# Optimization experiments

Measured on AMD Instinct MI355X. Metric: run time of the kernel, lower is better.

## Reference

```python
import jax, jax.numpy as jnp
from jax import lax
import numpy as np

B, T, N = 32, 1024, 128


def setup_inputs() -> dict:
    key = jax.random.key(0)
    k1, k2, k3 = jax.random.split(key, 3)
    x = jax.random.normal(k1, (B, T, N), dtype=jnp.float32)
    w_init = jax.random.normal(k2, (B, N, N), dtype=jnp.float32)
    mask = jax.random.randint(k3, (B, T), 0, 2, dtype=jnp.int32)
    alpha = jnp.float32(0.9)
    eta = jnp.float32(0.01)
    return {"x": x, "w_init": w_init, "alpha": alpha, "eta": eta, "mask": mask}


def reference(x, w_init, alpha, eta, mask):
    # x: (B,T,N), w_init: (B,N,N), mask: (B,T) int {0,1}
    maskf = mask.astype(x.dtype)

    def step(w, inp):
        xt, mt = inp                       # (B,N), (B,)
        yt = jnp.einsum('bij,bj->bi', w, xt)           # read-out with OLD w
        outer = xt[:, :, None] * xt[:, None, :]        # (B,N,N) Hebbian outer product
        w_new = alpha * w + eta * outer                # decay + Hebbian update
        m = mt[:, None, None]
        w = m * w_new + (1.0 - m) * w                  # masked update
        return w, yt

    xs = jnp.swapaxes(x, 0, 1)     # (T,B,N)
    ms = jnp.swapaxes(maskf, 0, 1) # (T,B)
    w_final, ys = lax.scan(step, w_init, (xs, ms))
    y_seq = jnp.swapaxes(ys, 0, 1)  # (B,T,N)
    return w_final, y_seq
```

## Files before the change

kernel.cpp:

```cpp
#include <hip/hip_runtime.h>

#define BB 32
#define TT 1024
#define NN 128
#define YB 256

#define ROR_ADD(p, ctrl)                                                      \
  p += __int_as_float(__builtin_amdgcn_update_dpp(                            \
      0, __float_as_int(p), ctrl, 0xF, 0xF, true));
#define BCAST15_ADD(p)                                                        \
  p += __int_as_float(__builtin_amdgcn_update_dpp(                            \
      0, __float_as_int(p), 0x142, 0xF, 0xF, true));

__global__ __launch_bounds__(256)
void bdh_seq_kernel(const float* __restrict__ x,
                    const float* __restrict__ w_init,
                    const float* __restrict__ alpha_p,
                    const float* __restrict__ eta_p,
                    const int*   __restrict__ mask,
                    float* __restrict__ out)
{
    const int tid  = threadIdx.x;
    const int bidx = blockIdx.x;
    const int b      = bidx & 31;
    const int i_base = (bidx >> 5) << 3;
    const int rloc   = tid >> 5;
    const int i      = i_base + rloc;
    const int cg     = tid & 31;
    const int j0     = cg << 2;

    __shared__ float ybuf[YB][8];

    const float alpha = alpha_p[0];
    const float eta   = eta_p[0];

    const float* xb   = x + (size_t)b * TT * NN;
    const float* xcol = xb + j0;
    const int*   mb   = mask + b * TT;

    float* wout = out + ((size_t)b * NN + i) * NN + j0;
    float* yout = out + (size_t)BB * NN * NN + (size_t)b * TT * NN;

    float4 w = *reinterpret_cast<const float4*>(
        w_init + ((size_t)b * NN + i) * NN + j0);

    float4 XA = *reinterpret_cast<const float4*>(xcol + 0 * NN);
    float4 XB = *reinterpret_cast<const float4*>(xcol + 1 * NN);
    float4 XC = *reinterpret_cast<const float4*>(xcol + 2 * NN);
    float4 XD = *reinterpret_cast<const float4*>(xcol + 3 * NN);
    float xiA = xb[0 * NN + i], xiB = xb[1 * NN + i];
    float xiC = xb[2 * NN + i], xiD = xb[3 * NN + i];
    int   mA_ = mb[0], mB_ = mb[1], mC_ = mb[2], mD_ = mb[3];

#define STEP(tt, X, XI, MM, TNEXT)                                            \
  {                                                                           \
    const float aa = MM ? alpha : 1.0f;                                       \
    const float ci = (MM ? eta : 0.0f) * XI;                                  \
      \
    float p0 = fmaf(w.y, X.y, w.x * X.x);                                     \
    float p1 = fmaf(w.w, X.w, w.z * X.z);                                     \
    float p  = p0 + p1;                                                       \
                         \
    w.x = fmaf(aa, w.x, ci * X.x);                                            \
    w.y = fmaf(aa, w.y, ci * X.y);                                            \
    w.z = fmaf(aa, w.z, ci * X.z);                                            \
    w.w = fmaf(aa, w.w, ci * X.w);                                            \
         \
    {                                                                         \
      int tn = (TNEXT) < TT ? (TNEXT) : (TT - 1);                             \
      const float* pn = xb + (size_t)tn * NN;                                 \
      X  = *reinterpret_cast<const float4*>(pn + j0);                         \
      XI = pn[i];                                                             \
      MM = mb[tn];                                                            \
    }                                                                         \
            \
    ROR_ADD(p, 0x121);                                                        \
    ROR_ADD(p, 0x122);                                                        \
    ROR_ADD(p, 0x124);                                                        \
    ROR_ADD(p, 0x128);                                                        \
    BCAST15_ADD(p);                                                           \
      \
    if ((tid & 31) == 16) ybuf[(tt) & (YB - 1)][rloc] = p;                    \
  }

#pragma unroll 1
    for (int t = 0; t < TT; t += 4) {
        STEP(t + 0, XA, xiA, mA_, t + 4);
        STEP(t + 1, XB, xiB, mB_, t + 5);
        STEP(t + 2, XC, xiC, mC_, t + 6);
        STEP(t + 3, XD, xiD, mD_, t + 7);
        if ((t & (YB - 1)) == YB - 4) {
            __syncthreads();
            const int t0 = t + 4 - YB;
#pragma unroll
            for (int pass = 0; pass < 8; ++pass) {
                const int tq = (tid >> 3) + (pass << 5);
                const int il = tid & 7;
                yout[(size_t)(t0 + tq) * NN + i_base + il] = ybuf[tq][il];
            }
            __syncthreads();
        }
    }
#undef STEP

    *reinterpret_cast<float4*>(wout) = w;
}

extern "C" void kernel_launch(void* const* d_in, const int* in_sizes, int n_in,
                              void* d_out, int out_size, void* d_ws, size_t ws_size,
                              hipStream_t stream)
{
    const float* x      = (const float*)d_in[0];
    const float* w_init = (const float*)d_in[1];
    const float* alpha  = (const float*)d_in[2];
    const float* eta    = (const float*)d_in[3];
    const int*   mask   = (const int*)d_in[4];
    float*       out    = (float*)d_out;

    dim3 grid(512), block(256);
    hipLaunchKernelGGL(bdh_seq_kernel, grid, block, 0, stream,
                       x, w_init, alpha, eta, mask, out);
}
```

Baseline: 230.9 us.

## Double-buffer 8-step input groups and batch DPP reductions across 16 steps

Replaces the 4-deep per-step prefetch with two 8-timestep register buffers loaded as groups, with masks loaded as int4 vectors. The 16 per-step cross-lane reductions are deferred and interleaved, so independent DPP chains can hide each other's latency instead of serializing after each step. The cost is higher register pressure (two buffers of 8 float4 plus 16 partial sums), which may reduce occupancy.

```diff
diff --git a/kernel.cpp b/kernel.cpp
--- a/kernel.cpp
+++ b/kernel.cpp
@@ -34,9 +34,8 @@
     const float alpha = alpha_p[0];
     const float eta   = eta_p[0];
 
-    const float* xb   = x + (size_t)b * TT * NN;
-    const float* xcol = xb + j0;
-    const int*   mb   = mask + b * TT;
+    const float* xb = x + (size_t)b * TT * NN;
+    const int*   mb = mask + b * TT;
 
     float* wout = out + ((size_t)b * NN + i) * NN + j0;
     float* yout = out + (size_t)BB * NN * NN + (size_t)b * TT * NN;
@@ -44,54 +43,71 @@
     float4 w = *reinterpret_cast<const float4*>(
         w_init + ((size_t)b * NN + i) * NN + j0);
 
-    float4 XA = *reinterpret_cast<const float4*>(xcol + 0 * NN);
-    float4 XB = *reinterpret_cast<const float4*>(xcol + 1 * NN);
-    float4 XC = *reinterpret_cast<const float4*>(xcol + 2 * NN);
-    float4 XD = *reinterpret_cast<const float4*>(xcol + 3 * NN);
-    float xiA = xb[0 * NN + i], xiB = xb[1 * NN + i];
-    float xiC = xb[2 * NN + i], xiD = xb[3 * NN + i];
-    int   mA_ = mb[0], mB_ = mb[1], mC_ = mb[2], mD_ = mb[3];
+    float4 Xc[8], Xn[8];
+    float  xic[8], xin[8];
+    int    mc[8],  mn[8];
+    float  p[16];
 
-#define STEP(tt, X, XI, MM, TNEXT)                                            \
+#define LOADG(X, XI, M, tbase)                                                \
   {                                                                           \
-    const float aa = MM ? alpha : 1.0f;                                       \
-    const float ci = (MM ? eta : 0.0f) * XI;                                  \
-      \
-    float p0 = fmaf(w.y, X.y, w.x * X.x);                                     \
-    float p1 = fmaf(w.w, X.w, w.z * X.z);                                     \
-    float p  = p0 + p1;                                                       \
-                         \
-    w.x = fmaf(aa, w.x, ci * X.x);                                            \
-    w.y = fmaf(aa, w.y, ci * X.y);                                            \
-    w.z = fmaf(aa, w.z, ci * X.z);                                            \
-    w.w = fmaf(aa, w.w, ci * X.w);                                            \
-         \
-    {                                                                         \
-      int tn = (TNEXT) < TT ? (TNEXT) : (TT - 1);                             \
-      const float* pn = xb + (size_t)tn * NN;                                 \
-      X  = *reinterpret_cast<const float4*>(pn + j0);                         \
-      XI = pn[i];                                                             \
-      MM = mb[tn];                                                            \
+    const float* gp = xb + (size_t)(tbase) * NN;                              \
+    _Pragma("unroll")                                                         \
+    for (int k = 0; k < 8; ++k) {                                             \
+      X[k]  = *reinterpret_cast<const float4*>(gp + k * NN + j0);             \
+      XI[k] = gp[k * NN + i];                                                 \
     }                                                                         \
-            \
-    ROR_ADD(p, 0x121);                                                        \
-    ROR_ADD(p, 0x122);                                                        \
-    ROR_ADD(p, 0x124);                                                        \
-    ROR_ADD(p, 0x128);                                                        \
-    BCAST15_ADD(p);                                                           \
-      \
-    if ((tid & 31) == 16) ybuf[(tt) & (YB - 1)][rloc] = p;                    \
+    *reinterpret_cast<int4*>(&M[0]) =                                         \
+        *reinterpret_cast<const int4*>(mb + (tbase));                         \
+    *reinterpret_cast<int4*>(&M[4]) =                                         \
+        *reinterpret_cast<const int4*>(mb + (tbase) + 4);                     \
   }
 
+#define COMPG(X, XI, M, pbase)                                                \
+  {                                                                           \
+    _Pragma("unroll")                                                         \
+    for (int k = 0; k < 8; ++k) {                                             \
+      const float aa = M[k] ? alpha : 1.0f;                                   \
+      const float ci = (M[k] ? eta : 0.0f) * XI[k];                           \
+      float p0 = fmaf(w.y, X[k].y, w.x * X[k].x);                             \
+      float p1 = fmaf(w.w, X[k].w, w.z * X[k].z);                             \
+      p[(pbase) + k] = p0 + p1;                                               \
+      w.x = fmaf(aa, w.x, ci * X[k].x);                                       \
+      w.y = fmaf(aa, w.y, ci * X[k].y);                                       \
+      w.z = fmaf(aa, w.z, ci * X[k].z);                                       \
+      w.w = fmaf(aa, w.w, ci * X[k].w);                                       \
+    }                                                                         \
+  }
+
+    LOADG(Xc, xic, mc, 0);
+    LOADG(Xn, xin, mn, 8);
+
 #pragma unroll 1
-    for (int t = 0; t < TT; t += 4) {
-        STEP(t + 0, XA, xiA, mA_, t + 4);
-        STEP(t + 1, XB, xiB, mB_, t + 5);
-        STEP(t + 2, XC, xiC, mC_, t + 6);
-        STEP(t + 3, XD, xiD, mD_, t + 7);
-        if ((t & (YB - 1)) == YB - 4) {
+    for (int t = 0; t < TT; t += 16) {
+        COMPG(Xc, xic, mc, 0);
+        if (t + 16 < TT) LOADG(Xc, xic, mc, t + 16);
+        COMPG(Xn, xin, mn, 8);
+        if (t + 24 < TT) LOADG(Xn, xin, mn, t + 24);
+
+#pragma unroll
+        for (int k = 0; k < 16; ++k) { ROR_ADD(p[k], 0x121); }
+#pragma unroll
+        for (int k = 0; k < 16; ++k) { ROR_ADD(p[k], 0x122); }
+#pragma unroll
+        for (int k = 0; k < 16; ++k) { ROR_ADD(p[k], 0x124); }
+#pragma unroll
+        for (int k = 0; k < 16; ++k) { ROR_ADD(p[k], 0x128); }
+#pragma unroll
+        for (int k = 0; k < 16; ++k) { BCAST15_ADD(p[k]); }
+
+        if (cg == 16) {
+#pragma unroll
+            for (int k = 0; k < 16; ++k)
+                ybuf[(t + k) & (YB - 1)][rloc] = p[k];
+        }
+
+        if (((t + 16) & (YB - 1)) == 0) {
             __syncthreads();
-            const int t0 = t + 4 - YB;
+            const int t0 = t + 16 - YB;
 #pragma unroll
             for (int pass = 0; pass < 8; ++pass) {
                 const int tq = (tid >> 3) + (pass << 5);
@@ -101,7 +117,8 @@
             __syncthreads();
         }
     }
-#undef STEP
+#undef LOADG
+#undef COMPG
 
     *reinterpret_cast<float4*>(wout) = w;
 }
```

After: 185.1 us. 19.9% less time.
